# Kernel tuning notes

Hardware: AMD Instinct MI355X
Metric: run time of the kernel (lower is better)

Reference implementation:

```python
import jax, jax.numpy as jnp
import numpy as np

N = 100000   # nodes
E = 3200000  # edges (avg degree 32)
F = 10       # input features
H = 20       # hidden dim
G = 512      # graphs in batch
L = 2        # labels


def xavier(key, shape):
    fan_in, fan_out = shape[0], shape[1]
    a = jnp.sqrt(6.0 / (fan_in + fan_out))
    return jax.random.uniform(key, shape, jnp.float32, -a, a)


def setup_inputs() -> dict:
    key = jax.random.key(0)
    ks = jax.random.split(key, 12)
    x = jax.random.normal(ks[0], (N, F), jnp.float32)
    edge_index = jax.random.randint(ks[1], (2, E), 0, N, jnp.int64)
    batch = jnp.sort(jax.random.randint(ks[2], (N,), 0, G, jnp.int64))
    return {
        "x": x,
        "edge_index": edge_index,
        "batch": batch,
        # layer 1: F -> H
        "W_rel1": xavier(ks[3], (F, H)), "b1": jnp.zeros((H,), jnp.float32),
        "W_root1": xavier(ks[4], (F, H)),
        # layer 2: H -> H
        "W_rel2": xavier(ks[5], (H, H)), "b2": jnp.zeros((H,), jnp.float32),
        "W_root2": xavier(ks[6], (H, H)),
        # layer 3: H -> H
        "W_rel3": xavier(ks[7], (H, H)), "b3": jnp.zeros((H,), jnp.float32),
        "W_root3": xavier(ks[8], (H, H)),
        # readout linear: 2H -> L
        "W_lin": xavier(ks[9], (2 * H, L)), "b_lin": jnp.zeros((L,), jnp.float32),
    }


def _graph_conv(x, src, dst, W_rel, b, W_root):
    # PyG GraphConv: out = lin_rel(sum_{j->i} x_j) + lin_root(x_i)
    agg = jax.ops.segment_sum(x[src], dst, num_segments=N)  # [N, d_in]
    return agg @ W_rel + b + x @ W_root


def reference(x, edge_index, batch, W_rel1, b1, W_root1, W_rel2, b2, W_root2,
              W_rel3, b3, W_root3, W_lin, b_lin):
    src, dst = edge_index[0], edge_index[1]
    h = jax.nn.relu(_graph_conv(x, src, dst, W_rel1, b1, W_root1))
    h = jax.nn.relu(_graph_conv(h, src, dst, W_rel2, b2, W_root2))
    h = jax.nn.relu(_graph_conv(h, src, dst, W_rel3, b3, W_root3))  # [N, H]
    # global max / mean pool over graphs
    maxp = jax.ops.segment_max(h, batch, num_segments=G)            # [G, H]
    sump = jax.ops.segment_sum(h, batch, num_segments=G)            # [G, H]
    counts = jax.ops.segment_sum(jnp.ones((h.shape[0], 1), h.dtype), batch,
                                 num_segments=G)                    # [G, 1]
    nonempty = counts > 0
    maxp = jnp.where(nonempty, maxp, 0.0)
    meanp = sump / jnp.maximum(counts, 1.0)
    pooled = jnp.concatenate([maxp, meanp], axis=-1)                # [G, 2H]
    return pooled @ W_lin + b_lin
```

## Files before the change

### kernel.cpp

```cpp
#include <hip/hip_runtime.h>
#include <hip/hip_bf16.h>

#define NN 100000
#define FF 10
#define HH 20
#define GG 512
#define LL 2

#define NB 500
#define BNODES 200
#define CAP 7168
#define STASH 14
#define TILE 4096
#define SRC_BITS 17
#define SRC_MASK 0x1FFFFu

__device__ inline unsigned short f2bf(float f) {
  unsigned u = __float_as_uint(f);
  unsigned r = u + 0x7FFFu + ((u >> 16) & 1u);
  return (unsigned short)(r >> 16);
}
__device__ inline float bflo(unsigned u) { return __uint_as_float(u << 16); }
__device__ inline float bfhi(unsigned u) { return __uint_as_float(u & 0xFFFF0000u); }

__global__ __launch_bounds__(256) void cast_init_kernel(
    const float* __restrict__ x, unsigned short* __restrict__ xb,
    float* __restrict__ sump, int* __restrict__ maxp, float* __restrict__ cnt,
    int* __restrict__ cursor, int n) {
  int i = blockIdx.x * 256 + threadIdx.x;
  if (i < n) xb[i] = f2bf(x[i]);
  if (i < GG * HH) {
    sump[i] = 0.0f;
    maxp[i] = 0;
  }
  if (i < GG) cnt[i] = 0.0f;
  if (i < NB) cursor[i] = 0;
}

__global__ __launch_bounds__(256) void multisplit_kernel(
    const int* __restrict__ src, const int* __restrict__ dst,
    int* __restrict__ cursor, unsigned int* __restrict__ pay, int E) {
  __shared__ int lhist[NB];
  __shared__ int lofs[NB];
  __shared__ int gbase[NB];
  __shared__ int lcur[NB];
  __shared__ unsigned int sord[TILE];
  __shared__ unsigned short sdbk[TILE];
  __shared__ int ss[512];
  int t = threadIdx.x;
  for (int i = t; i < NB; i += 256) lhist[i] = 0;
  __syncthreads();

  int base = blockIdx.x * TILE;
  int count = E - base;
  if (count > TILE) count = TILE;

  for (int i = t; i < count; i += 256)
    atomicAdd(&lhist[dst[base + i] / BNODES], 1);
  __syncthreads();

  int own0 = (t < NB) ? lhist[t] : 0;
  int own1 = (t + 256 < NB) ? lhist[t + 256] : 0;
  ss[t] = own0;
  ss[t + 256] = own1;
  __syncthreads();
  for (int off = 1; off < 512; off <<= 1) {
    int a0 = (t >= off) ? ss[t - off] : 0;
    int a1 = (t + 256 >= off) ? ss[t + 256 - off] : 0;
    __syncthreads();
    ss[t] += a0;
    ss[t + 256] += a1;
    __syncthreads();
  }
  if (t < NB) {
    lofs[t] = ss[t] - own0;
    int bo = own0 ? atomicAdd(&cursor[t], own0) : 0;
    if (bo > CAP - own0) bo = CAP - own0;
    gbase[t] = t * CAP + bo;
    lcur[t] = 0;
  }
  if (t + 256 < NB) {
    lofs[t + 256] = ss[t + 256] - own1;
    int bo = own1 ? atomicAdd(&cursor[t + 256], own1) : 0;
    if (bo > CAP - own1) bo = CAP - own1;
    gbase[t + 256] = (t + 256) * CAP + bo;
    lcur[t + 256] = 0;
  }
  __syncthreads();

  for (int i = t; i < count; i += 256) {
    int e = base + i;
    int d = __builtin_nontemporal_load(dst + e);
    int s = __builtin_nontemporal_load(src + e);
    int bk = d / BNODES;
    int ld = d - bk * BNODES;
    int r = atomicAdd(&lcur[bk], 1);
    int slot = lofs[bk] + r;
    sord[slot] = ((unsigned)ld << SRC_BITS) | (unsigned)s;
    sdbk[slot] = (unsigned short)bk;
  }
  __syncthreads();

  for (int i = t; i < count; i += 256) {
    int bk = sdbk[i];
    pay[gbase[bk] + (i - lofs[bk])] = sord[i];
  }
}

template<int DIN>
__global__ __launch_bounds__(512) void bucket_layer_kernel(
    const unsigned int* __restrict__ pay, const int* __restrict__ cursor,
    const unsigned short* __restrict__ hin, const float* __restrict__ Wrel,
    const float* __restrict__ bias, const float* __restrict__ Wroot,
    unsigned short* __restrict__ hout) {
  constexpr int AST = (DIN == 10) ? 11 : 21;
  constexpr int CH = DIN / 5;
  __shared__ int sSrc[CAP];
  __shared__ float acc[BNODES * AST];
  __shared__ unsigned short roots[BNODES * DIN];
  __shared__ float sWrel[DIN * HH];
  __shared__ float sWroot[DIN * HH];
  __shared__ float sb[HH];
  __shared__ int lhist[BNODES];
  __shared__ int lcur[BNODES];
  __shared__ int sRofs[BNODES];
  __shared__ int sRend[BNODES];
  __shared__ int ss[256];
  int b = blockIdx.x;
  int t = threadIdx.x;
  int nbase = b * BNODES;

  for (int i = t; i < DIN * HH; i += 512) {
    sWrel[i] = Wrel[i];
    sWroot[i] = Wroot[i];
  }
  if (t < HH) sb[t] = bias[t];
  if (t < BNODES) lhist[t] = 0;
  {
    const unsigned* rs = (const unsigned*)(hin + (size_t)nbase * DIN);
    unsigned* rd = (unsigned*)roots;
    for (int i = t; i < BNODES * DIN / 2; i += 512) rd[i] = rs[i];
  }
  __syncthreads();

  int ecnt = cursor[b];
  if (ecnt > CAP) ecnt = CAP;
  const unsigned int* mypay = pay + (size_t)b * CAP;

  unsigned ps[STASH];
#pragma unroll
  for (int u = 0; u < STASH; u++) {
    int i = t + u * 512;
    if (i < ecnt) {
      unsigned p = mypay[i];
      ps[u] = p;
      atomicAdd(&lhist[p >> SRC_BITS], 1);
    }
  }
  __syncthreads();

  int own = (t < BNODES) ? lhist[t] : 0;
  if (t < 256) ss[t] = own;
  __syncthreads();
  for (int off = 1; off < 256; off <<= 1) {
    int a0 = (t < 256 && t >= off) ? ss[t - off] : 0;
    __syncthreads();
    if (t < 256) ss[t] += a0;
    __syncthreads();
  }
  if (t < BNODES) {
    int ex = ss[t] - own;
    sRofs[t] = ex;
    sRend[t] = ex + own;
    lcur[t] = 0;
  }
  __syncthreads();

#pragma unroll
  for (int u = 0; u < STASH; u++) {
    int i = t + u * 512;
    if (i < ecnt) {
      unsigned p = ps[u];
      int ld = p >> SRC_BITS;
      int r = atomicAdd(&lcur[ld], 1);
      sSrc[sRofs[ld] + r] = (int)(p & SRC_MASK);
    }
  }
  __syncthreads();

  for (int task = t; task < BNODES * 5; task += 512) {
    int ln = task / 5;
    int c = task - ln * 5;
    int k0 = sRofs[ln], k1 = sRend[ln];
    if (CH == 4) {
      float a0 = 0, a1 = 0, a2 = 0, a3 = 0;
      const unsigned short* xb = hin + c * 4;
      for (int k = k0; k < k1; k++) {
        int s = sSrc[k];
        uint2 u = *(const uint2*)(xb + (size_t)s * 20);
        a0 += bflo(u.x);
        a1 += bfhi(u.x);
        a2 += bflo(u.y);
        a3 += bfhi(u.y);
      }
      float* a = acc + ln * AST + c * 4;
      a[0] = a0; a[1] = a1; a[2] = a2; a[3] = a3;
    } else {
      float a0 = 0, a1 = 0;
      const unsigned short* xb = hin + c * 2;
      for (int k = k0; k < k1; k++) {
        int s = sSrc[k];
        unsigned u = *(const unsigned*)(xb + (size_t)s * 10);
        a0 += bflo(u);
        a1 += bfhi(u);
      }
      float* a = acc + ln * AST + c * 2;
      a[0] = a0; a[1] = a1;
    }
  }
  __syncthreads();

  for (int idx = t; idx < BNODES * HH; idx += 512) {
    int ln = idx / HH;
    int j = idx - ln * HH;
    const float* a = acc + ln * AST;
    const unsigned short* r = roots + ln * DIN;
    float v = sb[j];
#pragma unroll
    for (int f = 0; f < DIN; f++) {
      v += a[f] * sWrel[f * HH + j];
      v += bflo((unsigned)r[f]) * sWroot[f * HH + j];
    }
    hout[(size_t)nbase * HH + idx] = f2bf(fmaxf(v, 0.0f));
  }
}

__global__ __launch_bounds__(512) void bucket_layer_pool_kernel(
    const unsigned int* __restrict__ pay, const int* __restrict__ cursor,
    const unsigned short* __restrict__ hin, const float* __restrict__ Wrel,
    const float* __restrict__ bias, const float* __restrict__ Wroot,
    const int* __restrict__ batch, float* __restrict__ sump,
    int* __restrict__ maxp, float* __restrict__ cnt) {
  constexpr int DIN = 20;
  constexpr int AST = 21;
  __shared__ int sSrc[CAP];
  __shared__ float acc[BNODES * AST];
  __shared__ unsigned short roots[BNODES * DIN];
  __shared__ int sBatch[BNODES];
  __shared__ float sWrel[DIN * HH];
  __shared__ float sWroot[DIN * HH];
  __shared__ float sb[HH];
  __shared__ int lhist[BNODES];
  __shared__ int lcur[BNODES];
  __shared__ int sRofs[BNODES];
  __shared__ int sRend[BNODES];
  __shared__ int ss[256];
  int b = blockIdx.x;
  int t = threadIdx.x;
  int nbase = b * BNODES;

  for (int i = t; i < DIN * HH; i += 512) {
    sWrel[i] = Wrel[i];
    sWroot[i] = Wroot[i];
  }
  if (t < HH) sb[t] = bias[t];
  if (t < BNODES) {
    lhist[t] = 0;
    sBatch[t] = batch[nbase + t];
  }
  {
    const unsigned* rs = (const unsigned*)(hin + (size_t)nbase * DIN);
    unsigned* rd = (unsigned*)roots;
    for (int i = t; i < BNODES * DIN / 2; i += 512) rd[i] = rs[i];
  }
  __syncthreads();

  int ecnt = cursor[b];
  if (ecnt > CAP) ecnt = CAP;
  const unsigned int* mypay = pay + (size_t)b * CAP;

  unsigned ps[STASH];
#pragma unroll
  for (int u = 0; u < STASH; u++) {
    int i = t + u * 512;
    if (i < ecnt) {
      unsigned p = mypay[i];
      ps[u] = p;
      atomicAdd(&lhist[p >> SRC_BITS], 1);
    }
  }
  __syncthreads();

  int own = (t < BNODES) ? lhist[t] : 0;
  if (t < 256) ss[t] = own;
  __syncthreads();
  for (int off = 1; off < 256; off <<= 1) {
    int a0 = (t < 256 && t >= off) ? ss[t - off] : 0;
    __syncthreads();
    if (t < 256) ss[t] += a0;
    __syncthreads();
  }
  if (t < BNODES) {
    int ex = ss[t] - own;
    sRofs[t] = ex;
    sRend[t] = ex + own;
    lcur[t] = 0;
  }
  __syncthreads();

#pragma unroll
  for (int u = 0; u < STASH; u++) {
    int i = t + u * 512;
    if (i < ecnt) {
      unsigned p = ps[u];
      int ld = p >> SRC_BITS;
      int r = atomicAdd(&lcur[ld], 1);
      sSrc[sRofs[ld] + r] = (int)(p & SRC_MASK);
    }
  }
  __syncthreads();

  for (int task = t; task < BNODES * 5; task += 512) {
    int ln = task / 5;
    int c = task - ln * 5;
    int k0 = sRofs[ln], k1 = sRend[ln];
    float a0 = 0, a1 = 0, a2 = 0, a3 = 0;
    const unsigned short* xb = hin + c * 4;
    for (int k = k0; k < k1; k++) {
      int s = sSrc[k];
      uint2 u = *(const uint2*)(xb + (size_t)s * 20);
      a0 += bflo(u.x);
      a1 += bfhi(u.x);
      a2 += bflo(u.y);
      a3 += bfhi(u.y);
    }
    float* a = acc + ln * AST + c * 4;
    a[0] = a0; a[1] = a1; a[2] = a2; a[3] = a3;
  }
  __syncthreads();

  float vreg[8];
#pragma unroll
  for (int u = 0; u < 8; u++) {
    int idx = t + u * 512;
    if (idx < BNODES * HH) {
      int ln = idx / HH;
      int j = idx - ln * HH;
      const float* a = acc + ln * AST;
      const unsigned short* r = roots + ln * DIN;
      float v = sb[j];
#pragma unroll
      for (int f = 0; f < DIN; f++) {
        v += a[f] * sWrel[f * HH + j];
        v += bflo((unsigned)r[f]) * sWroot[f * HH + j];
      }
      vreg[u] = fmaxf(v, 0.0f);
    }
  }
  __syncthreads();
#pragma unroll
  for (int u = 0; u < 8; u++) {
    int idx = t + u * 512;
    if (idx < BNODES * HH) {
      int ln = idx / HH;
      int j = idx - ln * HH;
      acc[ln * AST + j] = vreg[u];
    }
  }
  __syncthreads();

  int g0 = sBatch[0];
  int g1 = sBatch[BNODES - 1];
  int ngr = g1 - g0 + 1;
  for (int it = t; it < ngr * HH; it += 512) {
    int gi = it / HH;
    int j = it - gi * HH;
    int g = g0 + gi;
    float s = 0.0f, m = 0.0f;
    int c = 0;
    for (int ln = 0; ln < BNODES; ln++) {
      if (sBatch[ln] == g) {
        float v = acc[ln * AST + j];
        s += v;
        m = fmaxf(m, v);
        c++;
      }
    }
    if (c) {
      atomicAdd(&sump[g * HH + j], s);
      atomicMax(&maxp[g * HH + j], __float_as_int(m));
      if (j == 0) atomicAdd(&cnt[g], (float)c);
    }
  }
}

__global__ __launch_bounds__(256) void readout_kernel(
    const float* __restrict__ sump, const int* __restrict__ maxp,
    const float* __restrict__ cnt, const float* __restrict__ Wlin,
    const float* __restrict__ blin, float* __restrict__ out) {
  int idx = blockIdx.x * 256 + threadIdx.x;
  if (idx >= GG * LL) return;
  int g = idx / LL;
  int l = idx - g * LL;
  float c = cnt[g];
  float inv = 1.0f / fmaxf(c, 1.0f);
  float acc = blin[l];
#pragma unroll
  for (int j = 0; j < HH; j++) {
    float mx = __int_as_float(maxp[g * HH + j]);
    float mean = sump[g * HH + j] * inv;
    acc += mx * Wlin[j * LL + l];
    acc += mean * Wlin[(HH + j) * LL + l];
  }
  out[idx] = acc;
}

extern "C" void kernel_launch(void* const* d_in, const int* in_sizes, int n_in,
                              void* d_out, int out_size, void* d_ws,
                              size_t ws_size, hipStream_t stream) {
  const float* x = (const float*)d_in[0];
  const int* edge_index = (const int*)d_in[1];
  const int* batch = (const int*)d_in[2];
  const float* W_rel1 = (const float*)d_in[3];
  const float* b1 = (const float*)d_in[4];
  const float* W_root1 = (const float*)d_in[5];
  const float* W_rel2 = (const float*)d_in[6];
  const float* b2 = (const float*)d_in[7];
  const float* W_root2 = (const float*)d_in[8];
  const float* W_rel3 = (const float*)d_in[9];
  const float* b3 = (const float*)d_in[10];
  const float* W_root3 = (const float*)d_in[11];
  const float* W_lin = (const float*)d_in[12];
  const float* b_lin = (const float*)d_in[13];
  float* out = (float*)d_out;

  const int E = in_sizes[1] / 2;
  const int n_nodes = in_sizes[0] / FF;
  const int* src = edge_index;
  const int* dst = edge_index + E;

  unsigned int* pay = (unsigned int*)d_ws;
  int* cursor = (int*)(pay + (size_t)NB * CAP);
  float* sump = (float*)(cursor + 512);
  int* maxp = (int*)(sump + GG * HH);
  float* cnt = (float*)(maxp + GG * HH);
  unsigned short* xb = (unsigned short*)(cnt + 512);
  unsigned short* h1 = xb + (size_t)NN * FF;
  unsigned short* h2 = h1 + (size_t)NN * HH;

  const int edge_tiles = (E + TILE - 1) / TILE;

  cast_init_kernel<<<(n_nodes * FF + 255) / 256, 256, 0, stream>>>(
      x, xb, sump, maxp, cnt, cursor, n_nodes * FF);

  multisplit_kernel<<<edge_tiles, 256, 0, stream>>>(src, dst, cursor, pay, E);

  bucket_layer_kernel<FF><<<NB, 512, 0, stream>>>(
      pay, cursor, xb, W_rel1, b1, W_root1, h1);
  bucket_layer_kernel<HH><<<NB, 512, 0, stream>>>(
      pay, cursor, h1, W_rel2, b2, W_root2, h2);
  bucket_layer_pool_kernel<<<NB, 512, 0, stream>>>(
      pay, cursor, h2, W_rel3, b3, W_root3, batch, sump, maxp, cnt);

  readout_kernel<<<(GG * LL + 255) / 256, 256, 0, stream>>>(
      sump, maxp, cnt, W_lin, b_lin, out);
}
```

Before: 270.8 us.

## Drop cast kernel, gather fp32 input directly, process two nodes per thread

Removes the separate bf16 cast/init kernel: layer 1 now reads the fp32 input directly (float2 gathers), and zeroing moves to a single hipMemsetAsync. The gather loop is restructured so each of 500 threads handles two nodes (ln and ln+100) in an interleaved loop, giving more independent loads in flight per thread. This saves a launch and a full pass over x, at the cost of doubled read bytes for layer-1 gathers and load imbalance when the two nodes' degrees differ.

```diff
diff --git a/kernel.cpp b/kernel.cpp
--- a/kernel.cpp
+++ b/kernel.cpp
@@ -22,20 +22,6 @@
 }
 __device__ inline float bflo(unsigned u) { return __uint_as_float(u << 16); }
 __device__ inline float bfhi(unsigned u) { return __uint_as_float(u & 0xFFFF0000u); }
-
-__global__ __launch_bounds__(256) void cast_init_kernel(
-    const float* __restrict__ x, unsigned short* __restrict__ xb,
-    float* __restrict__ sump, int* __restrict__ maxp, float* __restrict__ cnt,
-    int* __restrict__ cursor, int n) {
-  int i = blockIdx.x * 256 + threadIdx.x;
-  if (i < n) xb[i] = f2bf(x[i]);
-  if (i < GG * HH) {
-    sump[i] = 0.0f;
-    maxp[i] = 0;
-  }
-  if (i < GG) cnt[i] = 0.0f;
-  if (i < NB) cursor[i] = 0;
-}
 
 __global__ __launch_bounds__(256) void multisplit_kernel(
     const int* __restrict__ src, const int* __restrict__ dst,
@@ -107,17 +93,18 @@
   }
 }
 
-template<int DIN>
+template<int DIN, bool F32IN>
 __global__ __launch_bounds__(512) void bucket_layer_kernel(
-    const unsigned int* __restrict__ pay, const int* __restrict__ cursor,
-    const unsigned short* __restrict__ hin, const float* __restrict__ Wrel,
+    const void* __restrict__ hin_v, const unsigned int* __restrict__ pay,
+    const int* __restrict__ cursor, const float* __restrict__ Wrel,
     const float* __restrict__ bias, const float* __restrict__ Wroot,
     unsigned short* __restrict__ hout) {
   constexpr int AST = (DIN == 10) ? 11 : 21;
   constexpr int CH = DIN / 5;
   __shared__ int sSrc[CAP];
   __shared__ float acc[BNODES * AST];
-  __shared__ unsigned short roots[BNODES * DIN];
+  __shared__ float rootsF[F32IN ? BNODES * DIN : 1];
+  __shared__ unsigned short rootsB[F32IN ? 1 : BNODES * DIN];
   __shared__ float sWrel[DIN * HH];
   __shared__ float sWroot[DIN * HH];
   __shared__ float sb[HH];
@@ -126,6 +113,8 @@
   __shared__ int sRofs[BNODES];
   __shared__ int sRend[BNODES];
   __shared__ int ss[256];
+  const float* hinF = (const float*)hin_v;
+  const unsigned short* hinB = (const unsigned short*)hin_v;
   int b = blockIdx.x;
   int t = threadIdx.x;
   int nbase = b * BNODES;
@@ -136,9 +125,12 @@
   }
   if (t < HH) sb[t] = bias[t];
   if (t < BNODES) lhist[t] = 0;
-  {
-    const unsigned* rs = (const unsigned*)(hin + (size_t)nbase * DIN);
-    unsigned* rd = (unsigned*)roots;
+  if (F32IN) {
+    const float* rs = hinF + (size_t)nbase * DIN;
+    for (int i = t; i < BNODES * DIN; i += 512) rootsF[i] = rs[i];
+  } else {
+    const unsigned* rs = (const unsigned*)(hinB + (size_t)nbase * DIN);
+    unsigned* rd = (unsigned*)rootsB;
     for (int i = t; i < BNODES * DIN / 2; i += 512) rd[i] = rs[i];
   }
   __syncthreads();
@@ -188,34 +180,67 @@
   }
   __syncthreads();
 
-  for (int task = t; task < BNODES * 5; task += 512) {
-    int ln = task / 5;
-    int c = task - ln * 5;
-    int k0 = sRofs[ln], k1 = sRend[ln];
+  if (t < 500) {
+    int lnA = t / 5;
+    int c = t - lnA * 5;
+    int lnB = lnA + 100;
+    int kA = sRofs[lnA], eA = sRend[lnA];
+    int kB = sRofs[lnB], eB = sRend[lnB];
+    int lenA = eA - kA, lenB = eB - kB;
+    int m = lenA < lenB ? lenA : lenB;
+    float a0A = 0, a1A = 0, a2A = 0, a3A = 0;
+    float a0B = 0, a1B = 0, a2B = 0, a3B = 0;
+    if (F32IN) {
+      const float* xb = hinF + c * CH;
+#pragma unroll 2
+      for (int i = 0; i < m; i++) {
+        int sA = sSrc[kA + i];
+        int sB = sSrc[kB + i];
+        float2 vA = *(const float2*)(xb + (size_t)sA * DIN);
+        float2 vB = *(const float2*)(xb + (size_t)sB * DIN);
+        a0A += vA.x; a1A += vA.y;
+        a0B += vB.x; a1B += vB.y;
+      }
+      for (int i = m; i < lenA; i++) {
+        float2 v = *(const float2*)(xb + (size_t)sSrc[kA + i] * DIN);
+        a0A += v.x; a1A += v.y;
+      }
+      for (int i = m; i < lenB; i++) {
+        float2 v = *(const float2*)(xb + (size_t)sSrc[kB + i] * DIN);
+        a0B += v.x; a1B += v.y;
+      }
+    } else {
+      const unsigned short* xb = hinB + c * CH;
+#pragma unroll 2
+      for (int i = 0; i < m; i++) {
+        int sA = sSrc[kA + i];
+        int sB = sSrc[kB + i];
+        uint2 uA = *(const uint2*)(xb + (size_t)sA * DIN);
+        uint2 uB = *(const uint2*)(xb + (size_t)sB * DIN);
+        a0A += bflo(uA.x); a1A += bfhi(uA.x);
+        a2A += bflo(uA.y); a3A += bfhi(uA.y);
+        a0B += bflo(uB.x); a1B += bfhi(uB.x);
+        a2B += bflo(uB.y); a3B += bfhi(uB.y);
+      }
+      for (int i = m; i < lenA; i++) {
+        uint2 u = *(const uint2*)(xb + (size_t)sSrc[kA + i] * DIN);
+        a0A += bflo(u.x); a1A += bfhi(u.x);
+        a2A += bflo(u.y); a3A += bfhi(u.y);
+      }
+      for (int i = m; i < lenB; i++) {
+        uint2 u = *(const uint2*)(xb + (size_t)sSrc[kB + i] * DIN);
+        a0B += bflo(u.x); a1B += bfhi(u.x);
+        a2B += bflo(u.y); a3B += bfhi(u.y);
+      }
+    }
+    float* aA = acc + lnA * AST + c * CH;
+    float* aB = acc + lnB * AST + c * CH;
     if (CH == 4) {
-      float a0 = 0, a1 = 0, a2 = 0, a3 = 0;
-      const unsigned short* xb = hin + c * 4;
-      for (int k = k0; k < k1; k++) {
-        int s = sSrc[k];
-        uint2 u = *(const uint2*)(xb + (size_t)s * 20);
-        a0 += bflo(u.x);
-        a1 += bfhi(u.x);
-        a2 += bflo(u.y);
-        a3 += bfhi(u.y);
-      }
-      float* a = acc + ln * AST + c * 4;
-      a[0] = a0; a[1] = a1; a[2] = a2; a[3] = a3;
+      aA[0] = a0A; aA[1] = a1A; aA[2] = a2A; aA[3] = a3A;
+      aB[0] = a0B; aB[1] = a1B; aB[2] = a2B; aB[3] = a3B;
     } else {
-      float a0 = 0, a1 = 0;
-      const unsigned short* xb = hin + c * 2;
-      for (int k = k0; k < k1; k++) {
-        int s = sSrc[k];
-        unsigned u = *(const unsigned*)(xb + (size_t)s * 10);
-        a0 += bflo(u);
-        a1 += bfhi(u);
-      }
-      float* a = acc + ln * AST + c * 2;
-      a[0] = a0; a[1] = a1;
+      aA[0] = a0A; aA[1] = a1A;
+      aB[0] = a0B; aB[1] = a1B;
     }
   }
   __syncthreads();
@@ -224,20 +249,20 @@
     int ln = idx / HH;
     int j = idx - ln * HH;
     const float* a = acc + ln * AST;
-    const unsigned short* r = roots + ln * DIN;
     float v = sb[j];
 #pragma unroll
     for (int f = 0; f < DIN; f++) {
+      float rv = F32IN ? rootsF[ln * DIN + f] : bflo((unsigned)rootsB[ln * DIN + f]);
       v += a[f] * sWrel[f * HH + j];
-      v += bflo((unsigned)r[f]) * sWroot[f * HH + j];
+      v += rv * sWroot[f * HH + j];
     }
     hout[(size_t)nbase * HH + idx] = f2bf(fmaxf(v, 0.0f));
   }
 }
 
 __global__ __launch_bounds__(512) void bucket_layer_pool_kernel(
-    const unsigned int* __restrict__ pay, const int* __restrict__ cursor,
-    const unsigned short* __restrict__ hin, const float* __restrict__ Wrel,
+    const unsigned short* __restrict__ hin, const unsigned int* __restrict__ pay,
+    const int* __restrict__ cursor, const float* __restrict__ Wrel,
     const float* __restrict__ bias, const float* __restrict__ Wroot,
     const int* __restrict__ batch, float* __restrict__ sump,
     int* __restrict__ maxp, float* __restrict__ cnt) {
@@ -320,22 +345,42 @@
   }
   __syncthreads();
 
-  for (int task = t; task < BNODES * 5; task += 512) {
-    int ln = task / 5;
-    int c = task - ln * 5;
-    int k0 = sRofs[ln], k1 = sRend[ln];
-    float a0 = 0, a1 = 0, a2 = 0, a3 = 0;
+  if (t < 500) {
+    int lnA = t / 5;
+    int c = t - lnA * 5;
+    int lnB = lnA + 100;
+    int kA = sRofs[lnA], eA = sRend[lnA];
+    int kB = sRofs[lnB], eB = sRend[lnB];
+    int lenA = eA - kA, lenB = eB - kB;
+    int m = lenA < lenB ? lenA : lenB;
+    float a0A = 0, a1A = 0, a2A = 0, a3A = 0;
+    float a0B = 0, a1B = 0, a2B = 0, a3B = 0;
     const unsigned short* xb = hin + c * 4;
-    for (int k = k0; k < k1; k++) {
-      int s = sSrc[k];
-      uint2 u = *(const uint2*)(xb + (size_t)s * 20);
-      a0 += bflo(u.x);
-      a1 += bfhi(u.x);
-      a2 += bflo(u.y);
-      a3 += bfhi(u.y);
-    }
-    float* a = acc + ln * AST + c * 4;
-    a[0] = a0; a[1] = a1; a[2] = a2; a[3] = a3;
+#pragma unroll 2
+    for (int i = 0; i < m; i++) {
+      int sA = sSrc[kA + i];
+      int sB = sSrc[kB + i];
+      uint2 uA = *(const uint2*)(xb + (size_t)sA * 20);
+      uint2 uB = *(const uint2*)(xb + (size_t)sB * 20);
+      a0A += bflo(uA.x); a1A += bfhi(uA.x);
+      a2A += bflo(uA.y); a3A += bfhi(uA.y);
+      a0B += bflo(uB.x); a1B += bfhi(uB.x);
+      a2B += bflo(uB.y); a3B += bfhi(uB.y);
+    }
+    for (int i = m; i < lenA; i++) {
+      uint2 u = *(const uint2*)(xb + (size_t)sSrc[kA + i] * 20);
+      a0A += bflo(u.x); a1A += bfhi(u.x);
+      a2A += bflo(u.y); a3A += bfhi(u.y);
+    }
+    for (int i = m; i < lenB; i++) {
+      uint2 u = *(const uint2*)(xb + (size_t)sSrc[kB + i] * 20);
+      a0B += bflo(u.x); a1B += bfhi(u.x);
+      a2B += bflo(u.y); a3B += bfhi(u.y);
+    }
+    float* aA = acc + lnA * AST + c * 4;
+    float* aB = acc + lnB * AST + c * 4;
+    aA[0] = a0A; aA[1] = a1A; aA[2] = a2A; aA[3] = a3A;
+    aB[0] = a0B; aB[1] = a1B; aB[2] = a2B; aB[3] = a3B;
   }
   __syncthreads();
 
@@ -436,6 +481,7 @@
 
   const int E = in_sizes[1] / 2;
   const int n_nodes = in_sizes[0] / FF;
+  (void)n_nodes;
   const int* src = edge_index;
   const int* dst = edge_index + E;
 
@@ -444,23 +490,22 @@
   float* sump = (float*)(cursor + 512);
   int* maxp = (int*)(sump + GG * HH);
   float* cnt = (float*)(maxp + GG * HH);
-  unsigned short* xb = (unsigned short*)(cnt + 512);
-  unsigned short* h1 = xb + (size_t)NN * FF;
+  unsigned short* h1 = (unsigned short*)(cnt + 512);
   unsigned short* h2 = h1 + (size_t)NN * HH;
 
   const int edge_tiles = (E + TILE - 1) / TILE;
 
-  cast_init_kernel<<<(n_nodes * FF + 255) / 256, 256, 0, stream>>>(
-      x, xb, sump, maxp, cnt, cursor, n_nodes * FF);
+  hipMemsetAsync(cursor, 0, (size_t)(512 + 2 * GG * HH + 512) * sizeof(int),
+                 stream);
 
   multisplit_kernel<<<edge_tiles, 256, 0, stream>>>(src, dst, cursor, pay, E);
 
-  bucket_layer_kernel<FF><<<NB, 512, 0, stream>>>(
-      pay, cursor, xb, W_rel1, b1, W_root1, h1);
-  bucket_layer_kernel<HH><<<NB, 512, 0, stream>>>(
-      pay, cursor, h1, W_rel2, b2, W_root2, h2);
+  bucket_layer_kernel<FF, true><<<NB, 512, 0, stream>>>(
+      x, pay, cursor, W_rel1, b1, W_root1, h1);
+  bucket_layer_kernel<HH, false><<<NB, 512, 0, stream>>>(
+      h1, pay, cursor, W_rel2, b2, W_root2, h2);
   bucket_layer_pool_kernel<<<NB, 512, 0, stream>>>(
-      pay, cursor, h2, W_rel3, b3, W_root3, batch, sump, maxp, cnt);
+      h2, pay, cursor, W_rel3, b3, W_root3, batch, sump, maxp, cnt);
 
   readout_kernel<<<(GG * LL + 255) / 256, 256, 0, stream>>>(
       sump, maxp, cnt, W_lin, b_lin, out);
```

Result: no change. 273.8 us (+1.1%).

## Split buckets across two blocks, read fp32 input directly, replace init kernel with memset

Applied to the files above, without the earlier changes.

Each 200-node bucket is now handled by two 100-node blocks that each scan the full bucket payload and keep only their half. This doubles the grid and cuts shared memory per block, which should raise occupancy. The first layer now gathers fp32 x directly, so the cast kernel goes away, and the zero-initialisation becomes a single hipMemsetAsync. The multisplit kernel moves to 512 threads. The cost is that every payload entry is read twice from global memory and layer-1 gathers move twice the bytes. The register stash is dropped, so payload words are re-read between the histogram and scatter passes.

```diff
diff --git a/kernel.cpp b/kernel.cpp
--- a/kernel.cpp
+++ b/kernel.cpp
@@ -10,7 +10,8 @@
 #define NB 500
 #define BNODES 200
 #define CAP 7168
-#define STASH 14
+#define HB 100
+#define SCAP 3712
 #define TILE 4096
 #define SRC_BITS 17
 #define SRC_MASK 0x1FFFFu
@@ -23,21 +24,7 @@
 __device__ inline float bflo(unsigned u) { return __uint_as_float(u << 16); }
 __device__ inline float bfhi(unsigned u) { return __uint_as_float(u & 0xFFFF0000u); }
 
-__global__ __launch_bounds__(256) void cast_init_kernel(
-    const float* __restrict__ x, unsigned short* __restrict__ xb,
-    float* __restrict__ sump, int* __restrict__ maxp, float* __restrict__ cnt,
-    int* __restrict__ cursor, int n) {
-  int i = blockIdx.x * 256 + threadIdx.x;
-  if (i < n) xb[i] = f2bf(x[i]);
-  if (i < GG * HH) {
-    sump[i] = 0.0f;
-    maxp[i] = 0;
-  }
-  if (i < GG) cnt[i] = 0.0f;
-  if (i < NB) cursor[i] = 0;
-}
-
-__global__ __launch_bounds__(256) void multisplit_kernel(
+__global__ __launch_bounds__(512) void multisplit_kernel(
     const int* __restrict__ src, const int* __restrict__ dst,
     int* __restrict__ cursor, unsigned int* __restrict__ pay, int E) {
   __shared__ int lhist[NB];
@@ -48,47 +35,36 @@
   __shared__ unsigned short sdbk[TILE];
   __shared__ int ss[512];
   int t = threadIdx.x;
-  for (int i = t; i < NB; i += 256) lhist[i] = 0;
+  if (t < NB) lhist[t] = 0;
   __syncthreads();
 
   int base = blockIdx.x * TILE;
   int count = E - base;
   if (count > TILE) count = TILE;
 
-  for (int i = t; i < count; i += 256)
+  for (int i = t; i < count; i += 512)
     atomicAdd(&lhist[dst[base + i] / BNODES], 1);
   __syncthreads();
 
-  int own0 = (t < NB) ? lhist[t] : 0;
-  int own1 = (t + 256 < NB) ? lhist[t + 256] : 0;
-  ss[t] = own0;
-  ss[t + 256] = own1;
+  int own = (t < NB) ? lhist[t] : 0;
+  ss[t] = own;
   __syncthreads();
   for (int off = 1; off < 512; off <<= 1) {
     int a0 = (t >= off) ? ss[t - off] : 0;
-    int a1 = (t + 256 >= off) ? ss[t + 256 - off] : 0;
     __syncthreads();
     ss[t] += a0;
-    ss[t + 256] += a1;
     __syncthreads();
   }
   if (t < NB) {
-    lofs[t] = ss[t] - own0;
-    int bo = own0 ? atomicAdd(&cursor[t], own0) : 0;
-    if (bo > CAP - own0) bo = CAP - own0;
+    lofs[t] = ss[t] - own;
+    int bo = own ? atomicAdd(&cursor[t], own) : 0;
+    if (bo > CAP - own) bo = CAP - own;
     gbase[t] = t * CAP + bo;
     lcur[t] = 0;
   }
-  if (t + 256 < NB) {
-    lofs[t + 256] = ss[t + 256] - own1;
-    int bo = own1 ? atomicAdd(&cursor[t + 256], own1) : 0;
-    if (bo > CAP - own1) bo = CAP - own1;
-    gbase[t + 256] = (t + 256) * CAP + bo;
-    lcur[t + 256] = 0;
-  }
-  __syncthreads();
-
-  for (int i = t; i < count; i += 256) {
+  __syncthreads();
+
+  for (int i = t; i < count; i += 512) {
     int e = base + i;
     int d = __builtin_nontemporal_load(dst + e);
     int s = __builtin_nontemporal_load(src + e);
@@ -101,234 +77,230 @@
   }
   __syncthreads();
 
-  for (int i = t; i < count; i += 256) {
+  for (int i = t; i < count; i += 512) {
     int bk = sdbk[i];
     pay[gbase[bk] + (i - lofs[bk])] = sord[i];
   }
 }
 
-template<int DIN>
+template<int DIN, bool F32IN>
 __global__ __launch_bounds__(512) void bucket_layer_kernel(
-    const unsigned int* __restrict__ pay, const int* __restrict__ cursor,
-    const unsigned short* __restrict__ hin, const float* __restrict__ Wrel,
+    const void* __restrict__ hin_v, const unsigned int* __restrict__ pay,
+    const int* __restrict__ cursor, const float* __restrict__ Wrel,
     const float* __restrict__ bias, const float* __restrict__ Wroot,
     unsigned short* __restrict__ hout) {
   constexpr int AST = (DIN == 10) ? 11 : 21;
   constexpr int CH = DIN / 5;
-  __shared__ int sSrc[CAP];
-  __shared__ float acc[BNODES * AST];
-  __shared__ unsigned short roots[BNODES * DIN];
+  __shared__ int sSrc[SCAP];
+  __shared__ float acc[HB * AST];
+  __shared__ float rootsF[F32IN ? HB * DIN : 1];
+  __shared__ unsigned short rootsB[F32IN ? 1 : HB * DIN];
   __shared__ float sWrel[DIN * HH];
   __shared__ float sWroot[DIN * HH];
   __shared__ float sb[HH];
-  __shared__ int lhist[BNODES];
-  __shared__ int lcur[BNODES];
-  __shared__ int sRofs[BNODES];
-  __shared__ int sRend[BNODES];
-  __shared__ int ss[256];
-  int b = blockIdx.x;
+  __shared__ int lhist[HB];
+  __shared__ int lcur[HB];
+  __shared__ int sRofs[HB];
+  __shared__ int sRend[HB];
+  __shared__ int ss[128];
+  const float* hinF = (const float*)hin_v;
+  const unsigned short* hinB = (const unsigned short*)hin_v;
+  int b2 = blockIdx.x;
+  int bucket = b2 >> 1;
+  int lo = (b2 & 1) * HB;
   int t = threadIdx.x;
-  int nbase = b * BNODES;
+  int nbase = b2 * HB;
 
   for (int i = t; i < DIN * HH; i += 512) {
     sWrel[i] = Wrel[i];
     sWroot[i] = Wroot[i];
   }
   if (t < HH) sb[t] = bias[t];
-  if (t < BNODES) lhist[t] = 0;
-  {
-    const unsigned* rs = (const unsigned*)(hin + (size_t)nbase * DIN);
-    unsigned* rd = (unsigned*)roots;
-    for (int i = t; i < BNODES * DIN / 2; i += 512) rd[i] = rs[i];
-  }
-  __syncthreads();
-
-  int ecnt = cursor[b];
+  if (t < HB) lhist[t] = 0;
+  if (F32IN) {
+    const float* rs = hinF + (size_t)nbase * DIN;
+    for (int i = t; i < HB * DIN; i += 512) rootsF[i] = rs[i];
+  } else {
+    const unsigned* rs = (const unsigned*)(hinB + (size_t)nbase * DIN);
+    unsigned* rd = (unsigned*)rootsB;
+    for (int i = t; i < HB * DIN / 2; i += 512) rd[i] = rs[i];
+  }
+  __syncthreads();
+
+  int ecnt = cursor[bucket];
   if (ecnt > CAP) ecnt = CAP;
-  const unsigned int* mypay = pay + (size_t)b * CAP;
-
-  unsigned ps[STASH];
-#pragma unroll
-  for (int u = 0; u < STASH; u++) {
-    int i = t + u * 512;
-    if (i < ecnt) {
-      unsigned p = mypay[i];
-      ps[u] = p;
-      atomicAdd(&lhist[p >> SRC_BITS], 1);
-    }
-  }
-  __syncthreads();
-
-  int own = (t < BNODES) ? lhist[t] : 0;
-  if (t < 256) ss[t] = own;
-  __syncthreads();
-  for (int off = 1; off < 256; off <<= 1) {
-    int a0 = (t < 256 && t >= off) ? ss[t - off] : 0;
-    __syncthreads();
-    if (t < 256) ss[t] += a0;
-    __syncthreads();
-  }
-  if (t < BNODES) {
+  const unsigned int* mypay = pay + (size_t)bucket * CAP;
+
+  for (int i = t; i < ecnt; i += 512) {
+    int ld = (int)(mypay[i] >> SRC_BITS) - lo;
+    if ((unsigned)ld < HB) atomicAdd(&lhist[ld], 1);
+  }
+  __syncthreads();
+
+  int own = (t < HB) ? lhist[t] : 0;
+  if (t < 128) ss[t] = own;
+  __syncthreads();
+  for (int off = 1; off < 128; off <<= 1) {
+    int a0 = (t < 128 && t >= off) ? ss[t - off] : 0;
+    __syncthreads();
+    if (t < 128) ss[t] += a0;
+    __syncthreads();
+  }
+  if (t < HB) {
     int ex = ss[t] - own;
     sRofs[t] = ex;
-    sRend[t] = ex + own;
+    int en = ex + own;
+    sRend[t] = en < SCAP ? en : SCAP;
     lcur[t] = 0;
   }
   __syncthreads();
 
-#pragma unroll
-  for (int u = 0; u < STASH; u++) {
-    int i = t + u * 512;
-    if (i < ecnt) {
-      unsigned p = ps[u];
-      int ld = p >> SRC_BITS;
+  for (int i = t; i < ecnt; i += 512) {
+    unsigned p = mypay[i];
+    int ld = (int)(p >> SRC_BITS) - lo;
+    if ((unsigned)ld < HB) {
       int r = atomicAdd(&lcur[ld], 1);
-      sSrc[sRofs[ld] + r] = (int)(p & SRC_MASK);
-    }
-  }
-  __syncthreads();
-
-  for (int task = t; task < BNODES * 5; task += 512) {
-    int ln = task / 5;
-    int c = task - ln * 5;
+      int slot = sRofs[ld] + r;
+      if (slot < SCAP) sSrc[slot] = (int)(p & SRC_MASK);
+    }
+  }
+  __syncthreads();
+
+  if (t < HB * 5) {
+    int ln = t / 5;
+    int c = t - ln * 5;
     int k0 = sRofs[ln], k1 = sRend[ln];
-    if (CH == 4) {
-      float a0 = 0, a1 = 0, a2 = 0, a3 = 0;
-      const unsigned short* xb = hin + c * 4;
+    float a0 = 0, a1 = 0, a2 = 0, a3 = 0;
+    if (F32IN) {
+      const float* xb = hinF + c * CH;
       for (int k = k0; k < k1; k++) {
-        int s = sSrc[k];
-        uint2 u = *(const uint2*)(xb + (size_t)s * 20);
+        float2 v = *(const float2*)(xb + (size_t)sSrc[k] * DIN);
+        a0 += v.x;
+        a1 += v.y;
+      }
+    } else {
+      const unsigned short* xb = hinB + c * CH;
+      for (int k = k0; k < k1; k++) {
+        uint2 u = *(const uint2*)(xb + (size_t)sSrc[k] * DIN);
         a0 += bflo(u.x);
         a1 += bfhi(u.x);
         a2 += bflo(u.y);
         a3 += bfhi(u.y);
       }
-      float* a = acc + ln * AST + c * 4;
+    }
+    float* a = acc + ln * AST + c * CH;
+    if (CH == 4) {
       a[0] = a0; a[1] = a1; a[2] = a2; a[3] = a3;
     } else {
-      float a0 = 0, a1 = 0;
-      const unsigned short* xb = hin + c * 2;
-      for (int k = k0; k < k1; k++) {
-        int s = sSrc[k];
-        unsigned u = *(const unsigned*)(xb + (size_t)s * 10);
-        a0 += bflo(u);
-        a1 += bfhi(u);
-      }
-      float* a = acc + ln * AST + c * 2;
       a[0] = a0; a[1] = a1;
     }
   }
   __syncthreads();
 
-  for (int idx = t; idx < BNODES * HH; idx += 512) {
+  for (int idx = t; idx < HB * HH; idx += 512) {
     int ln = idx / HH;
     int j = idx - ln * HH;
     const float* a = acc + ln * AST;
-    const unsigned short* r = roots + ln * DIN;
     float v = sb[j];
 #pragma unroll
     for (int f = 0; f < DIN; f++) {
+      float rv = F32IN ? rootsF[ln * DIN + f] : bflo((unsigned)rootsB[ln * DIN + f]);
       v += a[f] * sWrel[f * HH + j];
-      v += bflo((unsigned)r[f]) * sWroot[f * HH + j];
+      v += rv * sWroot[f * HH + j];
     }
     hout[(size_t)nbase * HH + idx] = f2bf(fmaxf(v, 0.0f));
   }
 }
 
 __global__ __launch_bounds__(512) void bucket_layer_pool_kernel(
-    const unsigned int* __restrict__ pay, const int* __restrict__ cursor,
-    const unsigned short* __restrict__ hin, const float* __restrict__ Wrel,
+    const unsigned short* __restrict__ hin, const unsigned int* __restrict__ pay,
+    const int* __restrict__ cursor, const float* __restrict__ Wrel,
     const float* __restrict__ bias, const float* __restrict__ Wroot,
     const int* __restrict__ batch, float* __restrict__ sump,
     int* __restrict__ maxp, float* __restrict__ cnt) {
   constexpr int DIN = 20;
   constexpr int AST = 21;
-  __shared__ int sSrc[CAP];
-  __shared__ float acc[BNODES * AST];
-  __shared__ unsigned short roots[BNODES * DIN];
-  __shared__ int sBatch[BNODES];
+  __shared__ int sSrc[SCAP];
+  __shared__ float acc[HB * AST];
+  __shared__ unsigned short roots[HB * DIN];
+  __shared__ int sBatch[HB];
   __shared__ float sWrel[DIN * HH];
   __shared__ float sWroot[DIN * HH];
   __shared__ float sb[HH];
-  __shared__ int lhist[BNODES];
-  __shared__ int lcur[BNODES];
-  __shared__ int sRofs[BNODES];
-  __shared__ int sRend[BNODES];
-  __shared__ int ss[256];
-  int b = blockIdx.x;
+  __shared__ int lhist[HB];
+  __shared__ int lcur[HB];
+  __shared__ int sRofs[HB];
+  __shared__ int sRend[HB];
+  __shared__ int ss[128];
+  int b2 = blockIdx.x;
+  int bucket = b2 >> 1;
+  int lo = (b2 & 1) * HB;
   int t = threadIdx.x;
-  int nbase = b * BNODES;
+  int nbase = b2 * HB;
 
   for (int i = t; i < DIN * HH; i += 512) {
     sWrel[i] = Wrel[i];
     sWroot[i] = Wroot[i];
   }
   if (t < HH) sb[t] = bias[t];
-  if (t < BNODES) {
+  if (t < HB) {
     lhist[t] = 0;
     sBatch[t] = batch[nbase + t];
   }
   {
     const unsigned* rs = (const unsigned*)(hin + (size_t)nbase * DIN);
     unsigned* rd = (unsigned*)roots;
-    for (int i = t; i < BNODES * DIN / 2; i += 512) rd[i] = rs[i];
-  }
-  __syncthreads();
-
-  int ecnt = cursor[b];
+    for (int i = t; i < HB * DIN / 2; i += 512) rd[i] = rs[i];
+  }
+  __syncthreads();
+
+  int ecnt = cursor[bucket];
   if (ecnt > CAP) ecnt = CAP;
-  const unsigned int* mypay = pay + (size_t)b * CAP;
-
-  unsigned ps[STASH];
-#pragma unroll
-  for (int u = 0; u < STASH; u++) {
-    int i = t + u * 512;
-    if (i < ecnt) {
-      unsigned p = mypay[i];
-      ps[u] = p;
-      atomicAdd(&lhist[p >> SRC_BITS], 1);
-    }
-  }
-  __syncthreads();
-
-  int own = (t < BNODES) ? lhist[t] : 0;
-  if (t < 256) ss[t] = own;
-  __syncthreads();
-  for (int off = 1; off < 256; off <<= 1) {
-    int a0 = (t < 256 && t >= off) ? ss[t - off] : 0;
-    __syncthreads();
-    if (t < 256) ss[t] += a0;
-    __syncthreads();
-  }
-  if (t < BNODES) {
+  const unsigned int* mypay = pay + (size_t)bucket * CAP;
+
+  for (int i = t; i < ecnt; i += 512) {
+    int ld = (int)(mypay[i] >> SRC_BITS) - lo;
+    if ((unsigned)ld < HB) atomicAdd(&lhist[ld], 1);
+  }
+  __syncthreads();
+
+  int own = (t < HB) ? lhist[t] : 0;
+  if (t < 128) ss[t] = own;
+  __syncthreads();
+  for (int off = 1; off < 128; off <<= 1) {
+    int a0 = (t < 128 && t >= off) ? ss[t - off] : 0;
+    __syncthreads();
+    if (t < 128) ss[t] += a0;
+    __syncthreads();
+  }
+  if (t < HB) {
     int ex = ss[t] - own;
     sRofs[t] = ex;
-    sRend[t] = ex + own;
+    int en = ex + own;
+    sRend[t] = en < SCAP ? en : SCAP;
     lcur[t] = 0;
   }
   __syncthreads();
 
-#pragma unroll
-  for (int u = 0; u < STASH; u++) {
-    int i = t + u * 512;
-    if (i < ecnt) {
-      unsigned p = ps[u];
-      int ld = p >> SRC_BITS;
+  for (int i = t; i < ecnt; i += 512) {
+    unsigned p = mypay[i];
+    int ld = (int)(p >> SRC_BITS) - lo;
+    if ((unsigned)ld < HB) {
       int r = atomicAdd(&lcur[ld], 1);
-      sSrc[sRofs[ld] + r] = (int)(p & SRC_MASK);
-    }
-  }
-  __syncthreads();
-
-  for (int task = t; task < BNODES * 5; task += 512) {
-    int ln = task / 5;
-    int c = task - ln * 5;
+      int slot = sRofs[ld] + r;
+      if (slot < SCAP) sSrc[slot] = (int)(p & SRC_MASK);
+    }
+  }
+  __syncthreads();
+
+  if (t < HB * 5) {
+    int ln = t / 5;
+    int c = t - ln * 5;
     int k0 = sRofs[ln], k1 = sRend[ln];
     float a0 = 0, a1 = 0, a2 = 0, a3 = 0;
     const unsigned short* xb = hin + c * 4;
     for (int k = k0; k < k1; k++) {
-      int s = sSrc[k];
-      uint2 u = *(const uint2*)(xb + (size_t)s * 20);
+      uint2 u = *(const uint2*)(xb + (size_t)sSrc[k] * 20);
       a0 += bflo(u.x);
       a1 += bfhi(u.x);
       a2 += bflo(u.y);
@@ -339,11 +311,11 @@
   }
   __syncthreads();
 
-  float vreg[8];
+  float vreg[4];
 #pragma unroll
-  for (int u = 0; u < 8; u++) {
+  for (int u = 0; u < 4; u++) {
     int idx = t + u * 512;
-    if (idx < BNODES * HH) {
+    if (idx < HB * HH) {
       int ln = idx / HH;
       int j = idx - ln * HH;
       const float* a = acc + ln * AST;
@@ -359,9 +331,9 @@
   }
   __syncthreads();
 #pragma unroll
-  for (int u = 0; u < 8; u++) {
+  for (int u = 0; u < 4; u++) {
     int idx = t + u * 512;
-    if (idx < BNODES * HH) {
+    if (idx < HB * HH) {
       int ln = idx / HH;
       int j = idx - ln * HH;
       acc[ln * AST + j] = vreg[u];
@@ -370,7 +342,7 @@
   __syncthreads();
 
   int g0 = sBatch[0];
-  int g1 = sBatch[BNODES - 1];
+  int g1 = sBatch[HB - 1];
   int ngr = g1 - g0 + 1;
   for (int it = t; it < ngr * HH; it += 512) {
     int gi = it / HH;
@@ -378,7 +350,7 @@
     int g = g0 + gi;
     float s = 0.0f, m = 0.0f;
     int c = 0;
-    for (int ln = 0; ln < BNODES; ln++) {
+    for (int ln = 0; ln < HB; ln++) {
       if (sBatch[ln] == g) {
         float v = acc[ln * AST + j];
         s += v;
@@ -435,7 +407,6 @@
   float* out = (float*)d_out;
 
   const int E = in_sizes[1] / 2;
-  const int n_nodes = in_sizes[0] / FF;
   const int* src = edge_index;
   const int* dst = edge_index + E;
 
@@ -444,23 +415,22 @@
   float* sump = (float*)(cursor + 512);
   int* maxp = (int*)(sump + GG * HH);
   float* cnt = (float*)(maxp + GG * HH);
-  unsigned short* xb = (unsigned short*)(cnt + 512);
-  unsigned short* h1 = xb + (size_t)NN * FF;
+  unsigned short* h1 = (unsigned short*)(cnt + 512);
   unsigned short* h2 = h1 + (size_t)NN * HH;
 
   const int edge_tiles = (E + TILE - 1) / TILE;
 
-  cast_init_kernel<<<(n_nodes * FF + 255) / 256, 256, 0, stream>>>(
-      x, xb, sump, maxp, cnt, cursor, n_nodes * FF);
-
-  multisplit_kernel<<<edge_tiles, 256, 0, stream>>>(src, dst, cursor, pay, E);
-
-  bucket_layer_kernel<FF><<<NB, 512, 0, stream>>>(
-      pay, cursor, xb, W_rel1, b1, W_root1, h1);
-  bucket_layer_kernel<HH><<<NB, 512, 0, stream>>>(
-      pay, cursor, h1, W_rel2, b2, W_root2, h2);
-  bucket_layer_pool_kernel<<<NB, 512, 0, stream>>>(
-      pay, cursor, h2, W_rel3, b3, W_root3, batch, sump, maxp, cnt);
+  hipMemsetAsync(cursor, 0, (size_t)(512 + 2 * GG * HH + 512) * sizeof(int),
+                 stream);
+
+  multisplit_kernel<<<edge_tiles, 512, 0, stream>>>(src, dst, cursor, pay, E);
+
+  bucket_layer_kernel<FF, true><<<NB * 2, 512, 0, stream>>>(
+      x, pay, cursor, W_rel1, b1, W_root1, h1);
+  bucket_layer_kernel<HH, false><<<NB * 2, 512, 0, stream>>>(
+      h1, pay, cursor, W_rel2, b2, W_root2, h2);
+  bucket_layer_pool_kernel<<<NB * 2, 512, 0, stream>>>(
+      h2, pay, cursor, W_rel3, b3, W_root3, batch, sump, maxp, cnt);
 
   readout_kernel<<<(GG * LL + 255) / 256, 256, 0, stream>>>(
       sump, maxp, cnt, W_lin, b_lin, out);
```

Result: no change. 271.5 us (+0.2%).
